# Performance work log

Measured on AMD Instinct MI355X. Metric: run time of the kernel, lower is better.

Reference implementation:

```python
import jax, jax.numpy as jnp
import numpy as np

B, S, D = 8, 2048, 1024
G, V = 2, 320          # num_groups, codebook_size
DG = D // G            # 512, per-group codevector dim
DIVERSITY_WEIGHT = 0.1


def setup_inputs() -> dict:
    key = jax.random.key(0)
    k1, k2, k3, k4 = jax.random.split(key, 4)
    hidden_states = jax.random.normal(k1, (B, S, D), dtype=jnp.float32)
    W = jax.random.normal(k2, (G * V, D), dtype=jnp.float32)   # weight_proj weight (torch Linear layout)
    b = jax.random.normal(k3, (G * V,), dtype=jnp.float32)     # weight_proj bias
    codevectors = jax.random.normal(k4, (1, G * V, DG), dtype=jnp.float32)
    return {"hidden_states": hidden_states, "W": W, "b": b, "codevectors": codevectors}


def reference(hidden_states, W, b, codevectors):
    batch, seq, _ = hidden_states.shape
    n_tok = batch * seq
    # weight_proj: [B,S,D] -> [B,S,G*V]
    logits = jnp.einsum("bsd,vd->bsv", hidden_states, W) + b
    logits_flat = logits.reshape(n_tok * G, V)
    # eval path: hard argmax codevector selection
    codevector_idx = jnp.argmax(logits_flat, axis=-1)          # [n_tok*G]
    probs = jax.nn.one_hot(codevector_idx, V, dtype=logits.dtype)  # exact one-hot, [n_tok*G, V]
    probs_g = probs.reshape(n_tok, G, V)
    # perplexity over marginal code usage (mask_time_indices=None)
    marginal = probs_g.mean(axis=0)                            # [G, V]
    perplexity = jnp.exp(-jnp.sum(marginal * jnp.log(marginal + 1e-7), axis=-1)).sum()
    # codevector lookup: one-hot @ codebook == gather of row g*V + idx_g
    idx2 = codevector_idx.reshape(n_tok, G)                    # [n_tok, G]
    cb = codevectors.reshape(G * V, DG)
    rows = idx2 + jnp.arange(G, dtype=idx2.dtype) * V          # global codebook rows
    gathered = jnp.take(cb, rows, axis=0)                      # [n_tok, G, DG]
    out = gathered.reshape(batch, seq, G * DG)                 # [B, S, D]
    # faithful to original (buggy) reshape: view(batch, num_groups, seq)
    idx_out = codevector_idx.reshape(batch, G, seq)
    num_codevectors = G * V
    diversity_loss = (num_codevectors - perplexity) / num_codevectors * DIVERSITY_WEIGHT
    return out, idx_out, diversity_loss
```

## Files before the change

kernel.cpp:

```cpp
#include <hip/hip_runtime.h>
#include <hip/hip_bf16.h>
#include <math.h>
#include <stdint.h>

#define BATCH 8
#define SEQ   2048
#define DMODEL 1024
#define GROUPS 2
#define VOCAB 320
#define NOUT  (GROUPS*VOCAB)
#define DG    (DMODEL/GROUPS)
#define NTOK  (BATCH*SEQ)
#define NPAIR (NTOK*GROUPS)
#define NCHUNK 10

#define MARGIN 4.0f
#define NEG_INF (-3.0e38f)

typedef __attribute__((ext_vector_type(8))) short short8;
typedef __attribute__((ext_vector_type(8))) unsigned short ushort8;
typedef __attribute__((ext_vector_type(4))) float f32x4;

__device__ __forceinline__ unsigned short f2bf(float f) {
    __hip_bfloat16 h = __float2bfloat16(f);
    return *reinterpret_cast<unsigned short*>(&h);
}
__device__ __forceinline__ float bf2f(unsigned short u) {
    unsigned int x = ((unsigned int)u) << 16;
    return __uint_as_float(x);
}

__device__ __forceinline__ void async16(const void* gptr, const void* lptr) {
    __builtin_amdgcn_global_load_lds(
        (const __attribute__((address_space(1))) unsigned int*)(unsigned long long)(uintptr_t)gptr,
        (__attribute__((address_space(3))) unsigned int*)(unsigned int)(uintptr_t)lptr,
        16, 0, 0);
}

#define NX4 (NTOK*DMODEL/4)
#define NW4 (NOUT*DMODEL/4)
__global__ __launch_bounds__(256) void convert_kernel(
    const float* __restrict__ X, const float* __restrict__ W,
    unsigned short* __restrict__ Xb, unsigned short* __restrict__ Wb)
{
    int i = blockIdx.x * 256 + threadIdx.x;
    const float4* src;
    ushort4* dst;
    int j;
    if (i < NX4) { src = (const float4*)X; dst = (ushort4*)Xb; j = i; }
    else         { src = (const float4*)W; dst = (ushort4*)Wb; j = i - NX4; if (j >= NW4) return; }
    float4 v = src[j];
    ushort4 u;
    u.x = f2bf(v.x); u.y = f2bf(v.y); u.z = f2bf(v.z); u.w = f2bf(v.w);
    dst[j] = u;
}

__global__ __launch_bounds__(256) void gemm_bf16_kernel(
    const unsigned short* __restrict__ Xb,
    const unsigned short* __restrict__ Wb,
    const float* __restrict__ bias,
    unsigned short* __restrict__ logits,
    float* __restrict__ rec_m1,
    float* __restrict__ rec_m2,
    int*   __restrict__ rec_id)
{
    __shared__ __align__(16) unsigned short As[128 * 32];
    __shared__ __align__(16) unsigned short Bs[128 * 32];

    const int tid  = threadIdx.x;
    const int lane = tid & 63;
    const int wave = tid >> 6;

    const int bid  = blockIdx.x;
    const int wgid = (bid & 7) * 80 + (bid >> 3);
    const int m0 = (wgid / 5) * 128;
    const int n0 = (wgid % 5) * 128;

    const int wm = (wave & 1) * 64;
    const int wn = (wave >> 1) * 64;

    f32x4 acc[4][4];
    #pragma unroll
    for (int a = 0; a < 4; a++)
        #pragma unroll
        for (int b = 0; b < 4; b++)
            acc[a][b] = (f32x4)0.0f;

    int aoff[2], boff[2], loff[2];
    #pragma unroll
    for (int j = 0; j < 2; j++) {
        int p = tid + j * 256;
        int r = p >> 2, s = p & 3;
        int c = s ^ ((r >> 1) & 3);
        aoff[j] = (m0 + r) * DMODEL + c * 8;
        boff[j] = (n0 + r) * DMODEL + c * 8;
        loff[j] = p * 8;
    }

    int afrag[4], bfrag[4];
    {
        int rho = lane & 15, h = lane >> 4;
        #pragma unroll
        for (int mi = 0; mi < 4; mi++) {
            int r = wm + mi * 16 + rho;
            afrag[mi] = (4 * r + (h ^ ((r >> 1) & 3))) * 8;
            int rn = wn + mi * 16 + rho;
            bfrag[mi] = (4 * rn + (h ^ ((rn >> 1) & 3))) * 8;
        }
    }

    for (int k0 = 0; k0 < DMODEL; k0 += 32) {
        #pragma unroll
        for (int j = 0; j < 2; j++) {
            async16(Xb + aoff[j] + k0, As + loff[j]);
            async16(Wb + boff[j] + k0, Bs + loff[j]);
        }
        __syncthreads();

        short8 af[4], bf[4];
        #pragma unroll
        for (int i = 0; i < 4; i++) {
            af[i] = *(const short8*)&As[afrag[i]];
            bf[i] = *(const short8*)&Bs[bfrag[i]];
        }
        #pragma unroll
        for (int mi = 0; mi < 4; mi++)
            #pragma unroll
            for (int ni = 0; ni < 4; ni++)
                acc[mi][ni] = __builtin_amdgcn_mfma_f32_16x16x32_bf16(
                    af[mi], bf[ni], acc[mi][ni], 0, 0, 0);
        __syncthreads();
    }

    const int colb = n0 + wn + (lane & 15);
    const int rowb = m0 + wm + (lane >> 4) * 4;
    const int chunk = (n0 + wn) >> 6;
    float bv[4];
    #pragma unroll
    for (int ni = 0; ni < 4; ni++) bv[ni] = bias[colb + ni * 16];

    #pragma unroll
    for (int mi = 0; mi < 4; mi++) {
        #pragma unroll
        for (int p = 0; p < 4; p++) {
            const int row = rowb + mi * 16 + p;
            float m1 = acc[mi][0][p] + bv[0];
            float m2 = NEG_INF;
            int i1 = colb;
            logits[row * NOUT + colb] = f2bf(m1);
            #pragma unroll
            for (int ni = 1; ni < 4; ni++) {
                float v = acc[mi][ni][p] + bv[ni];
                logits[row * NOUT + colb + ni * 16] = f2bf(v);
                if (v > m1) { m2 = m1; m1 = v; i1 = colb + ni * 16; }
                else        { m2 = fmaxf(m2, v); }
            }
            #pragma unroll
            for (int off = 1; off < 16; off <<= 1) {
                float om1 = __shfl_xor(m1, off);
                float om2 = __shfl_xor(m2, off);
                int   oi  = __shfl_xor(i1, off);
                float nm2 = fmaxf(fmaxf(m2, om2), fminf(m1, om1));
                if (om1 > m1 || (om1 == m1 && oi < i1)) { m1 = om1; i1 = oi; }
                m2 = nm2;
            }
            if ((lane & 15) == 0) {
                rec_m1[row * NCHUNK + chunk] = m1;
                rec_m2[row * NCHUNK + chunk] = m2;
                rec_id[row * NCHUNK + chunk] = i1;
            }
        }
    }
}

__global__ __launch_bounds__(256) void finalize_kernel(
    const float* __restrict__ X, const float* __restrict__ W,
    const float* __restrict__ bias,
    const unsigned short* __restrict__ logits,
    const float* __restrict__ rec_m1, const float* __restrict__ rec_m2,
    const int* __restrict__ rec_id,
    const float* __restrict__ cb,
    float* __restrict__ out, float* __restrict__ out_idx)
{
    __shared__ int   lcol[64];
    __shared__ float lM[64];
    __shared__ int   lamb[64];
    __shared__ int   slcnt;

    const int tid   = threadIdx.x;
    const int lane  = tid & 63;
    const int wave  = tid >> 6;
    const int pair0 = blockIdx.x * 64;

    if (tid < 64) {
        const int pair  = pair0 + tid;
        const int token = pair >> 1;
        const int g     = pair & 1;
        const int base  = token * NCHUNK + g * 5;

        float m1[5], M;
        int cstar = 0;
        #pragma unroll
        for (int c = 0; c < 5; c++) m1[c] = rec_m1[base + c];
        M = m1[0];
        #pragma unroll
        for (int c = 1; c < 5; c++)
            if (m1[c] > M) { M = m1[c]; cstar = c; }
        const float m2s = rec_m2[base + cstar];

        const float thr = M - MARGIN;
        bool amb = (m2s >= thr);
        #pragma unroll
        for (int c = 0; c < 5; c++)
            if (c != cstar && m1[c] >= thr) amb = true;

        if (!amb) {
            const int gcol = rec_id[base + cstar];
            lcol[tid] = gcol;
            out_idx[pair] = (float)(gcol - g * VOCAB);
        } else {
            lM[tid] = M;
        }
        unsigned long long mask = __ballot(amb);
        if (amb) {
            int off = __popcll(mask & ((1ull << tid) - 1ull));
            lamb[off] = tid;
        }
        if (tid == 0) slcnt = (int)__popcll(mask);
    }
    __syncthreads();
    const int nloc = slcnt;

    for (int s = wave; s < nloc; s += 4) {
        const int lp    = lamb[s];
        const int pair  = pair0 + lp;
        const float M   = lM[lp];
        const int token = pair >> 1;
        const int g     = pair & 1;

        const float4* xr = (const float4*)(X + (size_t)token * DMODEL);
        float4 xv[4];
        #pragma unroll
        for (int q = 0; q < 4; q++) xv[q] = xr[lane + 64 * q];

        const unsigned short* lp_ = logits + token * NOUT + g * VOCAB;
        const bool have = (lane < 40);
        ushort8 u = (ushort8)0;
        if (have) u = *(const ushort8*)(lp_ + lane * 8);

        const float thr = M - MARGIN;
        float best = NEG_INF;
        int bestcol = 0;

        #pragma unroll
        for (int j = 0; j < 8; j++) {
            bool c = have && (bf2f(u[j]) >= thr);
            unsigned long long mask = __ballot(c);
            while (mask) {
                const int b = __ffsll((long long)mask) - 1;
                mask &= mask - 1;
                const int col = b * 8 + j;
                const float4* wr = (const float4*)(W + (size_t)(g * VOCAB + col) * DMODEL);
                float acc = 0.0f;
                #pragma unroll
                for (int q = 0; q < 4; q++) {
                    float4 bb = wr[lane + 64 * q];
                    acc = fmaf(xv[q].x, bb.x, acc);
                    acc = fmaf(xv[q].y, bb.y, acc);
                    acc = fmaf(xv[q].z, bb.z, acc);
                    acc = fmaf(xv[q].w, bb.w, acc);
                }
                #pragma unroll
                for (int off = 32; off >= 1; off >>= 1)
                    acc += __shfl_xor(acc, off);
                const float logit = acc + bias[g * VOCAB + col];
                if (logit > best || (logit == best && col < bestcol)) {
                    best = logit; bestcol = col;
                }
            }
        }
        if (lane == 0) {
            lcol[lp] = g * VOCAB + bestcol;
            out_idx[pair] = (float)bestcol;
        }
    }
    __syncthreads();

    #pragma unroll 4
    for (int i = 0; i < 32; i++) {
        const int token = pair0 / 2 + i;
        const int gg = tid >> 7;
        const float4* src = (const float4*)(cb + (size_t)lcol[i * 2 + gg] * DG);
        ((float4*)(out + (size_t)token * DMODEL))[tid] = src[tid & 127];
    }
}

__global__ __launch_bounds__(256) void diversity_kernel(
    const float* __restrict__ out_idx, float* __restrict__ out_scalar)
{
    __shared__ int lhist[NOUT];
    __shared__ float s0[256], s1[256];
    const int tid = threadIdx.x;
    for (int i = tid; i < NOUT; i += 256) lhist[i] = 0;
    __syncthreads();

    const float4* oi4 = (const float4*)out_idx;
    for (int i = tid; i < NPAIR / 4; i += 256) {
        float4 v = oi4[i];
        atomicAdd(&lhist[0 * VOCAB + (int)v.x], 1);
        atomicAdd(&lhist[1 * VOCAB + (int)v.y], 1);
        atomicAdd(&lhist[0 * VOCAB + (int)v.z], 1);
        atomicAdd(&lhist[1 * VOCAB + (int)v.w], 1);
    }
    __syncthreads();

    float a0 = 0.0f, a1 = 0.0f;
    for (int i = tid; i < NOUT; i += 256) {
        float m = (float)lhist[i] * (1.0f / (float)NTOK);
        float t = m * logf(m + 1e-7f);
        if (i < VOCAB) a0 += t; else a1 += t;
    }
    s0[tid] = a0; s1[tid] = a1;
    __syncthreads();
    for (int s = 128; s > 0; s >>= 1) {
        if (tid < s) { s0[tid] += s0[tid + s]; s1[tid] += s1[tid + s]; }
        __syncthreads();
    }
    if (tid == 0) {
        float perplexity = expf(-s0[0]) + expf(-s1[0]);
        *out_scalar = ((float)NOUT - perplexity) / (float)NOUT * 0.1f;
    }
}

extern "C" void kernel_launch(void* const* d_in, const int* in_sizes, int n_in,
                              void* d_out, int out_size, void* d_ws, size_t ws_size,
                              hipStream_t stream) {
    const float* X    = (const float*)d_in[0];
    const float* W    = (const float*)d_in[1];
    const float* bias = (const float*)d_in[2];
    const float* cb   = (const float*)d_in[3];

    float* out      = (float*)d_out;
    float* out_idx  = out + (size_t)NTOK * DMODEL;
    float* out_loss = out_idx + NPAIR;

    char* p = (char*)d_ws;
    unsigned short* Xb = (unsigned short*)p;      p += (size_t)NTOK * DMODEL * 2;
    unsigned short* Wb = (unsigned short*)p;      p += (size_t)NOUT * DMODEL * 2;
    unsigned short* logits = (unsigned short*)p;  p += (size_t)NTOK * NOUT * 2;
    float* rec_m1 = (float*)p;                    p += (size_t)NTOK * NCHUNK * 4;
    float* rec_m2 = (float*)p;                    p += (size_t)NTOK * NCHUNK * 4;
    int*   rec_id = (int*)p;                      p += (size_t)NTOK * NCHUNK * 4;

    convert_kernel<<<(NX4 + NW4) / 256, 256, 0, stream>>>(X, W, Xb, Wb);

    gemm_bf16_kernel<<<640, 256, 0, stream>>>(Xb, Wb, bias, logits,
                                              rec_m1, rec_m2, rec_id);

    finalize_kernel<<<NPAIR / 64, 256, 0, stream>>>(X, W, bias, logits,
                                                    rec_m1, rec_m2, rec_id,
                                                    cb, out, out_idx);

    diversity_kernel<<<1, 256, 0, stream>>>(out_idx, out_loss);
}
```

Measured before the change: 196.6 us.

## Fuse fp32-to-bf16 conversion into GEMM tile loads with register prefetch

```diff
diff --git a/kernel.cpp b/kernel.cpp
--- a/kernel.cpp
+++ b/kernel.cpp
@@ -30,34 +30,9 @@
     return __uint_as_float(x);
 }
 
-__device__ __forceinline__ void async16(const void* gptr, const void* lptr) {
-    __builtin_amdgcn_global_load_lds(
-        (const __attribute__((address_space(1))) unsigned int*)(unsigned long long)(uintptr_t)gptr,
-        (__attribute__((address_space(3))) unsigned int*)(unsigned int)(uintptr_t)lptr,
-        16, 0, 0);
-}
-
-#define NX4 (NTOK*DMODEL/4)
-#define NW4 (NOUT*DMODEL/4)
-__global__ __launch_bounds__(256) void convert_kernel(
-    const float* __restrict__ X, const float* __restrict__ W,
-    unsigned short* __restrict__ Xb, unsigned short* __restrict__ Wb)
-{
-    int i = blockIdx.x * 256 + threadIdx.x;
-    const float4* src;
-    ushort4* dst;
-    int j;
-    if (i < NX4) { src = (const float4*)X; dst = (ushort4*)Xb; j = i; }
-    else         { src = (const float4*)W; dst = (ushort4*)Wb; j = i - NX4; if (j >= NW4) return; }
-    float4 v = src[j];
-    ushort4 u;
-    u.x = f2bf(v.x); u.y = f2bf(v.y); u.z = f2bf(v.z); u.w = f2bf(v.w);
-    dst[j] = u;
-}
-
-__global__ __launch_bounds__(256) void gemm_bf16_kernel(
-    const unsigned short* __restrict__ Xb,
-    const unsigned short* __restrict__ Wb,
+__global__ __launch_bounds__(256) void gemm_fused_kernel(
+    const float* __restrict__ X,
+    const float* __restrict__ Wf,
     const float* __restrict__ bias,
     unsigned short* __restrict__ logits,
     float* __restrict__ rec_m1,
@@ -109,12 +84,40 @@
         }
     }
 
-    for (int k0 = 0; k0 < DMODEL; k0 += 32) {
-        #pragma unroll
-        for (int j = 0; j < 2; j++) {
-            async16(Xb + aoff[j] + k0, As + loff[j]);
-            async16(Wb + boff[j] + k0, Bs + loff[j]);
-        }
+    float4 a0_[2], a1_[2], b0_[2], b1_[2];
+
+    #define LOADF(T) do {                                               \
+        _Pragma("unroll")                                               \
+        for (int j = 0; j < 2; j++) {                                   \
+            a0_[j] = *(const float4*)(X  + aoff[j] + (T) * 32);         \
+            a1_[j] = *(const float4*)(X  + aoff[j] + (T) * 32 + 4);     \
+            b0_[j] = *(const float4*)(Wf + boff[j] + (T) * 32);         \
+            b1_[j] = *(const float4*)(Wf + boff[j] + (T) * 32 + 4);     \
+        }                                                               \
+    } while (0)
+
+    #define CVTWRITE() do {                                             \
+        _Pragma("unroll")                                               \
+        for (int j = 0; j < 2; j++) {                                   \
+            ushort8 ua, ub;                                             \
+            ua[0]=f2bf(a0_[j].x); ua[1]=f2bf(a0_[j].y);                 \
+            ua[2]=f2bf(a0_[j].z); ua[3]=f2bf(a0_[j].w);                 \
+            ua[4]=f2bf(a1_[j].x); ua[5]=f2bf(a1_[j].y);                 \
+            ua[6]=f2bf(a1_[j].z); ua[7]=f2bf(a1_[j].w);                 \
+            ub[0]=f2bf(b0_[j].x); ub[1]=f2bf(b0_[j].y);                 \
+            ub[2]=f2bf(b0_[j].z); ub[3]=f2bf(b0_[j].w);                 \
+            ub[4]=f2bf(b1_[j].x); ub[5]=f2bf(b1_[j].y);                 \
+            ub[6]=f2bf(b1_[j].z); ub[7]=f2bf(b1_[j].w);                 \
+            *(ushort8*)(As + loff[j]) = ua;                             \
+            *(ushort8*)(Bs + loff[j]) = ub;                             \
+        }                                                               \
+    } while (0)
+
+    LOADF(0);
+    for (int t = 0; t < DMODEL / 32; ++t) {
+        CVTWRITE();
+        if (t < DMODEL / 32 - 1)
+            LOADF(t + 1);
         __syncthreads();
 
         short8 af[4], bf[4];
@@ -131,6 +134,8 @@
                     af[mi], bf[ni], acc[mi][ni], 0, 0, 0);
         __syncthreads();
     }
+    #undef LOADF
+    #undef CVTWRITE
 
     const int colb = n0 + wn + (lane & 15);
     const int rowb = m0 + wm + (lane >> 4) * 4;
@@ -345,17 +350,13 @@
     float* out_loss = out_idx + NPAIR;
 
     char* p = (char*)d_ws;
-    unsigned short* Xb = (unsigned short*)p;      p += (size_t)NTOK * DMODEL * 2;
-    unsigned short* Wb = (unsigned short*)p;      p += (size_t)NOUT * DMODEL * 2;
     unsigned short* logits = (unsigned short*)p;  p += (size_t)NTOK * NOUT * 2;
     float* rec_m1 = (float*)p;                    p += (size_t)NTOK * NCHUNK * 4;
     float* rec_m2 = (float*)p;                    p += (size_t)NTOK * NCHUNK * 4;
     int*   rec_id = (int*)p;                      p += (size_t)NTOK * NCHUNK * 4;
 
-    convert_kernel<<<(NX4 + NW4) / 256, 256, 0, stream>>>(X, W, Xb, Wb);
-
-    gemm_bf16_kernel<<<640, 256, 0, stream>>>(Xb, Wb, bias, logits,
-                                              rec_m1, rec_m2, rec_id);
+    gemm_fused_kernel<<<640, 256, 0, stream>>>(X, W, bias, logits,
+                                               rec_m1, rec_m2, rec_id);
 
     finalize_kernel<<<NPAIR / 64, 256, 0, stream>>>(X, W, bias, logits,
                                                     rec_m1, rec_m2, rec_id,
```

Result: slower. 219.2 us (+11.5%).

## Fuse diversity histogram into finalize and widen GEMM K-step to 64

Applied to the files above, without the earlier changes.

```diff
diff --git a/kernel.cpp b/kernel.cpp
--- a/kernel.cpp
+++ b/kernel.cpp
@@ -41,9 +41,14 @@
 #define NW4 (NOUT*DMODEL/4)
 __global__ __launch_bounds__(256) void convert_kernel(
     const float* __restrict__ X, const float* __restrict__ W,
-    unsigned short* __restrict__ Xb, unsigned short* __restrict__ Wb)
+    unsigned short* __restrict__ Xb, unsigned short* __restrict__ Wb,
+    int* __restrict__ hist, int* __restrict__ done)
 {
     int i = blockIdx.x * 256 + threadIdx.x;
+    if (blockIdx.x == 0) {
+        for (int k = threadIdx.x; k < NOUT; k += 256) hist[k] = 0;
+        if (threadIdx.x == 0) *done = 0;
+    }
     const float4* src;
     ushort4* dst;
     int j;
@@ -64,8 +69,8 @@
     float* __restrict__ rec_m2,
     int*   __restrict__ rec_id)
 {
-    __shared__ __align__(16) unsigned short As[128 * 32];
-    __shared__ __align__(16) unsigned short Bs[128 * 32];
+    __shared__ __align__(16) unsigned short As[2][128 * 32];
+    __shared__ __align__(16) unsigned short Bs[2][128 * 32];
 
     const int tid  = threadIdx.x;
     const int lane = tid & 63;
@@ -109,26 +114,31 @@
         }
     }
 
-    for (int k0 = 0; k0 < DMODEL; k0 += 32) {
-        #pragma unroll
-        for (int j = 0; j < 2; j++) {
-            async16(Xb + aoff[j] + k0, As + loff[j]);
-            async16(Wb + boff[j] + k0, Bs + loff[j]);
-        }
+    for (int k0 = 0; k0 < DMODEL; k0 += 64) {
+        #pragma unroll
+        for (int h = 0; h < 2; h++)
+            #pragma unroll
+            for (int j = 0; j < 2; j++) {
+                async16(Xb + aoff[j] + k0 + h * 32, As[h] + loff[j]);
+                async16(Wb + boff[j] + k0 + h * 32, Bs[h] + loff[j]);
+            }
         __syncthreads();
 
-        short8 af[4], bf[4];
-        #pragma unroll
-        for (int i = 0; i < 4; i++) {
-            af[i] = *(const short8*)&As[afrag[i]];
-            bf[i] = *(const short8*)&Bs[bfrag[i]];
-        }
-        #pragma unroll
-        for (int mi = 0; mi < 4; mi++)
-            #pragma unroll
-            for (int ni = 0; ni < 4; ni++)
-                acc[mi][ni] = __builtin_amdgcn_mfma_f32_16x16x32_bf16(
-                    af[mi], bf[ni], acc[mi][ni], 0, 0, 0);
+        #pragma unroll
+        for (int h = 0; h < 2; h++) {
+            short8 af[4], bf[4];
+            #pragma unroll
+            for (int i = 0; i < 4; i++) {
+                af[i] = *(const short8*)&As[h][afrag[i]];
+                bf[i] = *(const short8*)&Bs[h][bfrag[i]];
+            }
+            #pragma unroll
+            for (int mi = 0; mi < 4; mi++)
+                #pragma unroll
+                for (int ni = 0; ni < 4; ni++)
+                    acc[mi][ni] = __builtin_amdgcn_mfma_f32_16x16x32_bf16(
+                        af[mi], bf[ni], acc[mi][ni], 0, 0, 0);
+        }
         __syncthreads();
     }
 
@@ -180,12 +190,16 @@
     const float* __restrict__ rec_m1, const float* __restrict__ rec_m2,
     const int* __restrict__ rec_id,
     const float* __restrict__ cb,
-    float* __restrict__ out, float* __restrict__ out_idx)
+    float* __restrict__ out, float* __restrict__ out_idx,
+    int* __restrict__ hist, int* __restrict__ done,
+    float* __restrict__ out_loss)
 {
     __shared__ int   lcol[64];
     __shared__ float lM[64];
     __shared__ int   lamb[64];
     __shared__ int   slcnt;
+    __shared__ int   lastFlag;
+    __shared__ float s0[256], s1[256];
 
     const int tid   = threadIdx.x;
     const int lane  = tid & 63;
@@ -218,6 +232,7 @@
             const int gcol = rec_id[base + cstar];
             lcol[tid] = gcol;
             out_idx[pair] = (float)(gcol - g * VOCAB);
+            atomicAdd(&hist[gcol], 1);
         } else {
             lM[tid] = M;
         }
@@ -280,10 +295,16 @@
             }
         }
         if (lane == 0) {
-            lcol[lp] = g * VOCAB + bestcol;
+            const int gcol = g * VOCAB + bestcol;
+            lcol[lp] = gcol;
             out_idx[pair] = (float)bestcol;
-        }
-    }
+            atomicAdd(&hist[gcol], 1);
+        }
+    }
+
+    __threadfence();
+    __syncthreads();
+    if (tid == 0) lastFlag = (atomicAdd(done, 1) == (int)gridDim.x - 1);
     __syncthreads();
 
     #pragma unroll 4
@@ -293,30 +314,13 @@
         const float4* src = (const float4*)(cb + (size_t)lcol[i * 2 + gg] * DG);
         ((float4*)(out + (size_t)token * DMODEL))[tid] = src[tid & 127];
     }
-}
-
-__global__ __launch_bounds__(256) void diversity_kernel(
-    const float* __restrict__ out_idx, float* __restrict__ out_scalar)
-{
-    __shared__ int lhist[NOUT];
-    __shared__ float s0[256], s1[256];
-    const int tid = threadIdx.x;
-    for (int i = tid; i < NOUT; i += 256) lhist[i] = 0;
-    __syncthreads();
-
-    const float4* oi4 = (const float4*)out_idx;
-    for (int i = tid; i < NPAIR / 4; i += 256) {
-        float4 v = oi4[i];
-        atomicAdd(&lhist[0 * VOCAB + (int)v.x], 1);
-        atomicAdd(&lhist[1 * VOCAB + (int)v.y], 1);
-        atomicAdd(&lhist[0 * VOCAB + (int)v.z], 1);
-        atomicAdd(&lhist[1 * VOCAB + (int)v.w], 1);
-    }
-    __syncthreads();
+
+    if (!lastFlag) return;
 
     float a0 = 0.0f, a1 = 0.0f;
     for (int i = tid; i < NOUT; i += 256) {
-        float m = (float)lhist[i] * (1.0f / (float)NTOK);
+        int h = atomicAdd(&hist[i], 0);
+        float m = (float)h * (1.0f / (float)NTOK);
         float t = m * logf(m + 1e-7f);
         if (i < VOCAB) a0 += t; else a1 += t;
     }
@@ -328,7 +332,7 @@
     }
     if (tid == 0) {
         float perplexity = expf(-s0[0]) + expf(-s1[0]);
-        *out_scalar = ((float)NOUT - perplexity) / (float)NOUT * 0.1f;
+        *out_loss = ((float)NOUT - perplexity) / (float)NOUT * 0.1f;
     }
 }
 
@@ -351,15 +355,17 @@
     float* rec_m1 = (float*)p;                    p += (size_t)NTOK * NCHUNK * 4;
     float* rec_m2 = (float*)p;                    p += (size_t)NTOK * NCHUNK * 4;
     int*   rec_id = (int*)p;                      p += (size_t)NTOK * NCHUNK * 4;
-
-    convert_kernel<<<(NX4 + NW4) / 256, 256, 0, stream>>>(X, W, Xb, Wb);
+    int* hist = (int*)p;                          p += NOUT * 4;
+    int* done = (int*)p;                          p += 256;
+
+    convert_kernel<<<(NX4 + NW4) / 256, 256, 0, stream>>>(X, W, Xb, Wb,
+                                                          hist, done);
 
     gemm_bf16_kernel<<<640, 256, 0, stream>>>(Xb, Wb, bias, logits,
                                               rec_m1, rec_m2, rec_id);
 
     finalize_kernel<<<NPAIR / 64, 256, 0, stream>>>(X, W, bias, logits,
                                                     rec_m1, rec_m2, rec_id,
-                                                    cb, out, out_idx);
-
-    diversity_kernel<<<1, 256, 0, stream>>>(out_idx, out_loss);
-}
+                                                    cb, out, out_idx,
+                                                    hist, done, out_loss);
+}
```

Measured after the change: 260.3 us. 1.32x slower.
